# Kernel optimization log

Hardware: AMD Instinct MI355X
Metric: run time of the kernel (lower is better)

Reference implementation:

```python
import jax, jax.numpy as jnp
import numpy as np

N, E, DIN, DOUT = 50000, 625000, 128, 128


def setup_inputs() -> dict:
    key = jax.random.key(0)
    k = jax.random.split(key, 4)
    x = jax.random.normal(k[0], (N, DIN), dtype=jnp.float32)
    edge_index = jax.random.randint(k[1], (2, E), 0, N, dtype=jnp.int32)
    s = 1.0 / np.sqrt(DIN)  # Glorot-ish init like torch Linear
    W_fwd = jax.random.uniform(k[2], (DIN, DOUT), jnp.float32, -s, s)
    W_bwd = jax.random.uniform(k[3], (DIN, DOUT), jnp.float32, -s, s)
    b_fwd = jnp.zeros((DOUT,), jnp.float32)
    b_bwd = jnp.zeros((DOUT,), jnp.float32)
    return {"x": x, "edge_index": edge_index, "W_fwd": W_fwd, "b_fwd": b_fwd,
            "W_bwd": W_bwd, "b_bwd": b_bwd}


def gcn_conv(x, W, b, src, dst, n):
    """PyG GCNConv: add self-loops, symmetric degree norm, gather-scatter aggregate."""
    loops = jnp.arange(n, dtype=src.dtype)
    src2 = jnp.concatenate([src, loops])  # [E+N]
    dst2 = jnp.concatenate([dst, loops])
    ones = jnp.ones(src2.shape[0], dtype=x.dtype)
    deg = jax.ops.segment_sum(ones, dst2, num_segments=n)  # in-degree incl. self-loop
    dinv = jnp.where(deg > 0, jax.lax.rsqrt(deg), 0.0)
    norm = dinv[src2] * dinv[dst2]  # [E+N]
    h = x @ W  # [N, DOUT] dense GEMM before message passing
    msgs = h[src2] * norm[:, None]  # gather + scale, [E+N, DOUT]
    out = jax.ops.segment_sum(msgs, dst2, num_segments=n)  # scatter-add
    return out + b


def reference(x, edge_index, W_fwd, b_fwd, W_bwd, b_bwd):
    src, dst = edge_index[0], edge_index[1]
    n = x.shape[0]
    x_forward = gcn_conv(x, W_fwd, b_fwd, src, dst, n)
    # reversed edge direction for the backward diffusion conv
    x_backward = gcn_conv(x, W_bwd, b_bwd, dst, src, n)
    # dropout omitted (eval mode / deterministic reference)
    return jax.nn.relu(x_forward + x_backward)
```

## Files before the change

kernel.cpp:

```cpp
#include <hip/hip_runtime.h>
#include <hip/hip_bf16.h>
#include <cstdint>

static constexpr int BLK      = 256;
static constexpr int CAP      = 40;
static constexpr int BINSHIFT = 8;
static constexpr int BINNODES = 1 << BINSHIFT;
static constexpr int BINCAP   = BINNODES * CAP / 2;
static constexpr int EPB      = 2048;
static constexpr int OVMAX    = 1024;

typedef __attribute__((ext_vector_type(8))) short bf16x8;
typedef __attribute__((ext_vector_type(4))) float f32x4;

__device__ __forceinline__ float bf16lo(uint32_t u) { return __uint_as_float(u << 16); }
__device__ __forceinline__ float bf16hi(uint32_t u) { return __uint_as_float(u & 0xffff0000u); }
__device__ __forceinline__ unsigned short f2bf(float f) {
    __hip_bfloat16 h = __float2bfloat16(f);
    return *(unsigned short*)&h;
}

__global__ __launch_bounds__(BLK) void k_prep(
        const float* __restrict__ Wf, const float* __restrict__ Wb,
        unsigned short* __restrict__ WTf, unsigned short* __restrict__ WTb,
        int* __restrict__ gcnt, int gcnt_words) {
    const int bid = blockIdx.x;
    if (bid < 8) {
        for (int idx = bid * 2048 + threadIdx.x; idx < (bid + 1) * 2048; idx += BLK) {
            int c = idx >> 7, k = idx & 127;
            WTf[c * 128 + k] = f2bf(Wf[k * 128 + c]);
            WTb[c * 128 + k] = f2bf(Wb[k * 128 + c]);
        }
        return;
    }
    for (int i = threadIdx.x; i < gcnt_words; i += BLK) gcnt[i] = 0;
}

__global__ __launch_bounds__(BLK) void k_bin_gemm(
        const int* __restrict__ src, const int* __restrict__ dst, int ne,
        uint32_t* __restrict__ pair_f, uint32_t* __restrict__ pair_b,
        int* __restrict__ gcnt_f, int* __restrict__ gcnt_b,
        int* __restrict__ ovcnt, int* __restrict__ ovlist,
        const float* __restrict__ x,
        const unsigned short* __restrict__ WTf,
        const unsigned short* __restrict__ WTb,
        unsigned short* __restrict__ h_f, unsigned short* __restrict__ h_b,
        int n, int nbins, int gbin) {
    const int bid = blockIdx.x;
    if (bid < gbin) {
        __shared__ int curf[BINNODES], curb[BINNODES];
        const int tid = threadIdx.x;
        curf[tid] = 0; curb[tid] = 0;
        __syncthreads();

        int s[8], d[8];
        const int e0 = bid * EPB + tid;
#pragma unroll
        for (int k = 0; k < 8; ++k) {
            int e = e0 + k * BLK;
            bool v = e < ne;
            s[k] = v ? src[e] : -1;
            d[k] = v ? dst[e] : -1;
            if (v) {
                atomicAdd(&curf[d[k] >> BINSHIFT], 1);
                atomicAdd(&curb[s[k] >> BINSHIFT], 1);
            }
        }
        __syncthreads();
        int cf = curf[tid], cb = curb[tid];
        if (tid < nbins) {
            curf[tid] = cf ? atomicAdd(&gcnt_f[tid], cf) : 0;
            curb[tid] = cb ? atomicAdd(&gcnt_b[tid], cb) : 0;
        }
        __syncthreads();
#pragma unroll
        for (int k = 0; k < 8; ++k) {
            if (s[k] >= 0) {
                int bf = d[k] >> BINSHIFT;
                int rf = atomicAdd(&curf[bf], 1);
                if (rf < BINCAP)
                    pair_f[(size_t)bf * BINCAP + rf] =
                        ((uint32_t)d[k] << 16) | (uint32_t)s[k];
                else { int q = atomicAdd(ovcnt, 1); if (q < OVMAX) ovlist[q] = (d[k] << 1) | 0; }
                int bb = s[k] >> BINSHIFT;
                int rb = atomicAdd(&curb[bb], 1);
                if (rb < BINCAP)
                    pair_b[(size_t)bb * BINCAP + rb] =
                        ((uint32_t)s[k] << 16) | (uint32_t)d[k];
                else { int q = atomicAdd(ovcnt, 1); if (q < OVMAX) ovlist[q] = (s[k] << 1) | 1; }
            }
        }
        return;
    }
    {
        const int gb   = bid - gbin;
        const int wave = threadIdx.x >> 6;
        const int lane = threadIdx.x & 63;
        const int conv = wave >> 1;
        const int n0   = (wave & 1) * 64;
        const int m0   = gb * 16;
        const int q    = lane >> 4;
        const int t16  = lane & 15;

        const unsigned short* __restrict__ WT = conv ? WTb : WTf;
        unsigned short* __restrict__ h        = conv ? h_b : h_f;

        int arow = m0 + t16; if (arow >= n) arow = n - 1;
        const float* __restrict__ xr = x + (size_t)arow * 128;
        bf16x8 a[4];
#pragma unroll
        for (int s2 = 0; s2 < 4; ++s2) {
            float4 p0v = *(const float4*)(xr + s2 * 32 + q * 8);
            float4 p1v = *(const float4*)(xr + s2 * 32 + q * 8 + 4);
            bf16x8 v;
            v[0] = (short)f2bf(p0v.x); v[1] = (short)f2bf(p0v.y);
            v[2] = (short)f2bf(p0v.z); v[3] = (short)f2bf(p0v.w);
            v[4] = (short)f2bf(p1v.x); v[5] = (short)f2bf(p1v.y);
            v[6] = (short)f2bf(p1v.z); v[7] = (short)f2bf(p1v.w);
            a[s2] = v;
        }
#pragma unroll
        for (int t = 0; t < 4; ++t) {
            const unsigned short* wrow = WT + (size_t)(n0 + t * 16 + t16) * 128;
            f32x4 c = {0.f, 0.f, 0.f, 0.f};
#pragma unroll
            for (int s2 = 0; s2 < 4; ++s2) {
                bf16x8 b = *(const bf16x8*)(wrow + s2 * 32 + q * 8);
                c = __builtin_amdgcn_mfma_f32_16x16x32_bf16(a[s2], b, c, 0, 0, 0);
            }
#pragma unroll
            for (int r = 0; r < 4; ++r) {
                int row = m0 + q * 4 + r;
                if (row < n)
                    h[(size_t)row * 128 + n0 + t * 16 + t16] = f2bf(c[r]);
            }
        }
    }
}

__global__ __launch_bounds__(BLK) void k_build(
        const uint32_t* __restrict__ pair_f, const uint32_t* __restrict__ pair_b,
        const int* __restrict__ gcnt_f, const int* __restrict__ gcnt_b,
        unsigned short* __restrict__ adj_f, unsigned short* __restrict__ adj_b,
        int* __restrict__ cnt_f, int* __restrict__ cnt_b,
        float* __restrict__ dinv_f, float* __restrict__ dinv_b,
        int* __restrict__ ovcnt, int* __restrict__ ovlist,
        int n, int nbins) {
    const int tid = threadIdx.x;
    const int b   = blockIdx.x;
    const int dir = b >= nbins ? 1 : 0;
    const int bin = b - dir * nbins;

    const uint32_t* __restrict__ pairs = dir ? pair_b : pair_f;
    unsigned short* __restrict__ adj   = dir ? adj_b : adj_f;
    int*   cnt  = dir ? cnt_b  : cnt_f;
    float* dinv = dir ? dinv_b : dinv_f;
    int count = dir ? gcnt_b[bin] : gcnt_f[bin];
    if (count > BINCAP) count = BINCAP;

    __shared__ unsigned short buck[BINNODES * CAP];
    __shared__ int lcnt[BINNODES];
    lcnt[tid] = 0;
    __syncthreads();

    const uint32_t* pb = pairs + (size_t)bin * BINCAP;
    for (int i = tid; i < count; i += BLK) {
        uint32_t p = pb[i];
        int l = (p >> 16) & (BINNODES - 1);
        int r = atomicAdd(&lcnt[l], 1);
        if (r < CAP) buck[l * CAP + r] = (unsigned short)(p & 0xffffu);
        else {
            int q = atomicAdd(ovcnt, 1);
            if (q < OVMAX) ovlist[q] = ((((bin << BINSHIFT) + l) << 1) | dir);
        }
    }
    __syncthreads();

    const int node0 = bin << BINSHIFT;
    const int node  = node0 + tid;
    if (node < n) {
        int c = lcnt[tid];
        cnt[node]  = c;
        dinv[node] = rsqrtf(1.0f + (float)c);
    }
    uint32_t* adjseg = (uint32_t*)(adj + (size_t)node0 * CAP);
    const uint32_t* b32 = (const uint32_t*)buck;
    for (int i = tid; i < BINCAP; i += BLK) adjseg[i] = b32[i];
}

__global__ __launch_bounds__(BLK) void k_gatherX(
        const int* __restrict__ cnt_f, const unsigned short* __restrict__ adj_f,
        const int* __restrict__ cnt_b, const unsigned short* __restrict__ adj_b,
        const float* __restrict__ dinv_f, const float* __restrict__ dinv_b,
        const uint32_t* __restrict__ hf, const uint32_t* __restrict__ hb,
        const float* __restrict__ bf, const float* __restrict__ bb,
        float* __restrict__ out, int n, int gnode, int nwords,
        const int* __restrict__ ovcnt, const int* __restrict__ ovlist,
        const int* __restrict__ src, const int* __restrict__ dst, int ne) {
    const int bid = blockIdx.x;
    if (bid < gnode) {
        const int wave = threadIdx.x >> 6;
        const int lane = threadIdx.x & 63;
        const int node = bid * 4 + wave;
        if (node >= n) return;

        int cf = cnt_f[node], cb = cnt_b[node];
        if (cf > CAP || cb > CAP) return;

        float dvsf = dinv_f[node], dvsb = dinv_b[node];
        uint32_t uf = hf[(size_t)node * 64 + lane];
        uint32_t ub = hf[(size_t)(nwords + node * 64 + lane)];
        float acc0 = dvsf * dvsf * bf16lo(uf) + dvsb * dvsb * bf16lo(ub);
        float acc1 = dvsf * dvsf * bf16hi(uf) + dvsb * dvsb * bf16hi(ub);

        const int mt = cf + cb;
        if (mt <= 64) {
            int ofs = 0; float sc = 0.f;
            if (lane < cf) {
                int nb = adj_f[node * CAP + lane];
                ofs = nb * 64;
                sc  = dvsf * dinv_f[nb];
            } else if (lane < mt) {
                int nb = adj_b[node * CAP + (lane - cf)];
                ofs = nwords + nb * 64;
                sc  = dvsb * dinv_b[nb];
            }
            int j = 0;
            for (; j + 8 <= mt; j += 8) {
                int   o0 = __shfl(ofs, j + 0), o1 = __shfl(ofs, j + 1);
                int   o2 = __shfl(ofs, j + 2), o3 = __shfl(ofs, j + 3);
                int   o4 = __shfl(ofs, j + 4), o5 = __shfl(ofs, j + 5);
                int   o6 = __shfl(ofs, j + 6), o7 = __shfl(ofs, j + 7);
                float s0 = __shfl(sc, j + 0), s1 = __shfl(sc, j + 1);
                float s2 = __shfl(sc, j + 2), s3 = __shfl(sc, j + 3);
                float s4 = __shfl(sc, j + 4), s5 = __shfl(sc, j + 5);
                float s6 = __shfl(sc, j + 6), s7 = __shfl(sc, j + 7);
                uint32_t u0 = hf[(size_t)(o0 + lane)];
                uint32_t u1 = hf[(size_t)(o1 + lane)];
                uint32_t u2 = hf[(size_t)(o2 + lane)];
                uint32_t u3 = hf[(size_t)(o3 + lane)];
                uint32_t u4 = hf[(size_t)(o4 + lane)];
                uint32_t u5 = hf[(size_t)(o5 + lane)];
                uint32_t u6 = hf[(size_t)(o6 + lane)];
                uint32_t u7 = hf[(size_t)(o7 + lane)];
                acc0 = fmaf(s0, bf16lo(u0), acc0); acc1 = fmaf(s0, bf16hi(u0), acc1);
                acc0 = fmaf(s1, bf16lo(u1), acc0); acc1 = fmaf(s1, bf16hi(u1), acc1);
                acc0 = fmaf(s2, bf16lo(u2), acc0); acc1 = fmaf(s2, bf16hi(u2), acc1);
                acc0 = fmaf(s3, bf16lo(u3), acc0); acc1 = fmaf(s3, bf16hi(u3), acc1);
                acc0 = fmaf(s4, bf16lo(u4), acc0); acc1 = fmaf(s4, bf16hi(u4), acc1);
                acc0 = fmaf(s5, bf16lo(u5), acc0); acc1 = fmaf(s5, bf16hi(u5), acc1);
                acc0 = fmaf(s6, bf16lo(u6), acc0); acc1 = fmaf(s6, bf16hi(u6), acc1);
                acc0 = fmaf(s7, bf16lo(u7), acc0); acc1 = fmaf(s7, bf16hi(u7), acc1);
            }
            for (; j + 4 <= mt; j += 4) {
                int   o0 = __shfl(ofs, j + 0), o1 = __shfl(ofs, j + 1);
                int   o2 = __shfl(ofs, j + 2), o3 = __shfl(ofs, j + 3);
                float s0 = __shfl(sc, j + 0), s1 = __shfl(sc, j + 1);
                float s2 = __shfl(sc, j + 2), s3 = __shfl(sc, j + 3);
                uint32_t u0 = hf[(size_t)(o0 + lane)];
                uint32_t u1 = hf[(size_t)(o1 + lane)];
                uint32_t u2 = hf[(size_t)(o2 + lane)];
                uint32_t u3 = hf[(size_t)(o3 + lane)];
                acc0 = fmaf(s0, bf16lo(u0), acc0); acc1 = fmaf(s0, bf16hi(u0), acc1);
                acc0 = fmaf(s1, bf16lo(u1), acc0); acc1 = fmaf(s1, bf16hi(u1), acc1);
                acc0 = fmaf(s2, bf16lo(u2), acc0); acc1 = fmaf(s2, bf16hi(u2), acc1);
                acc0 = fmaf(s3, bf16lo(u3), acc0); acc1 = fmaf(s3, bf16hi(u3), acc1);
            }
            for (; j < mt; ++j) {
                int oj = __shfl(ofs, j); float sj = __shfl(sc, j);
                uint32_t uj = hf[(size_t)(oj + lane)];
                acc0 = fmaf(sj, bf16lo(uj), acc0); acc1 = fmaf(sj, bf16hi(uj), acc1);
            }
        } else {
            for (int j = 0; j < cf; ++j) {
                int nb = adj_f[node * CAP + j];
                float dj = dvsf * dinv_f[nb];
                uint32_t u = hf[(size_t)nb * 64 + lane];
                acc0 = fmaf(dj, bf16lo(u), acc0); acc1 = fmaf(dj, bf16hi(u), acc1);
            }
            for (int j = 0; j < cb; ++j) {
                int nb = adj_b[node * CAP + j];
                float dj = dvsb * dinv_b[nb];
                uint32_t u = hf[(size_t)(nwords + nb * 64 + lane)];
                acc0 = fmaf(dj, bf16lo(u), acc0); acc1 = fmaf(dj, bf16hi(u), acc1);
            }
        }

        const float2 biasf = ((const float2*)bf)[lane];
        const float2 biasb = ((const float2*)bb)[lane];
        float v0 = acc0 + biasf.x + biasb.x;
        float v1 = acc1 + biasf.y + biasb.y;
        ((float2*)out)[(size_t)node * 64 + lane] =
            make_float2(fmaxf(v0, 0.0f), fmaxf(v1, 0.0f));
        return;
    }

    int nov = *ovcnt; if (nov > OVMAX) nov = OVMAX;
    if (nov == 0) return;
    __shared__ int lst[4096];
    __shared__ int lcnt;
    const int tid = threadIdx.x;
    for (int i = bid - gnode; i < nov; i += 8) {
        int code = ovlist[i];
        int node = code >> 1;
        float acc0 = 0.f, acc1 = 0.f;
        for (int d2 = 0; d2 < 2; ++d2) {
            const int* key = d2 ? src : dst;
            const int* val = d2 ? dst : src;
            const float* dinv = d2 ? dinv_b : dinv_f;
            int base = d2 ? nwords : 0;
            float dvs = dinv[node];
            float s0 = 0.f, s1 = 0.f;
            if (tid < 64) {
                uint32_t u = hf[(size_t)(base + node * 64 + tid)];
                s0 = dvs * bf16lo(u); s1 = dvs * bf16hi(u);
            }
            for (int start = 0; start < ne; start += 4096) {
                if (tid == 0) lcnt = 0;
                __syncthreads();
                int end = min(start + 4096, ne);
                for (int e2 = start + tid; e2 < end; e2 += BLK)
                    if (key[e2] == node) { int q = atomicAdd(&lcnt, 1); lst[q] = val[e2]; }
                __syncthreads();
                int mm = lcnt;
                if (tid < 64) {
                    for (int j = 0; j < mm; ++j) {
                        int nb = lst[j];
                        float dv = dinv[nb];
                        uint32_t u = hf[(size_t)(base + nb * 64 + tid)];
                        s0 = fmaf(dv, bf16lo(u), s0);
                        s1 = fmaf(dv, bf16hi(u), s1);
                    }
                }
                __syncthreads();
            }
            if (tid < 64) { acc0 += dvs * s0; acc1 += dvs * s1; }
        }
        if (tid < 64) {
            float2 biasf = ((const float2*)bf)[tid];
            float2 biasb = ((const float2*)bb)[tid];
            float v0 = acc0 + biasf.x + biasb.x;
            float v1 = acc1 + biasf.y + biasb.y;
            ((float2*)out)[(size_t)node * 64 + tid] =
                make_float2(fmaxf(v0, 0.0f), fmaxf(v1, 0.0f));
        }
        __syncthreads();
    }
}

extern "C" void kernel_launch(void* const* d_in, const int* in_sizes, int n_in,
                              void* d_out, int out_size, void* d_ws, size_t ws_size,
                              hipStream_t stream) {
    const float* x  = (const float*)d_in[0];
    const int*   ei = (const int*)d_in[1];
    const float* Wf = (const float*)d_in[2];
    const float* bf = (const float*)d_in[3];
    const float* Wb = (const float*)d_in[4];
    const float* bb = (const float*)d_in[5];

    const int n  = in_sizes[0] / 128;
    const int ne = in_sizes[1] / 2;
    const int* src = ei;
    const int* dst = ei + ne;
    float* out = (float*)d_out;

    const int nbins = (n + BINNODES - 1) >> BINSHIFT;

    char* w = (char*)d_ws;
    unsigned short* h_f = (unsigned short*)w;   w += (size_t)n * 128 * 2;
    unsigned short* h_b = (unsigned short*)w;   w += (size_t)n * 128 * 2;
    uint32_t* pair_f = (uint32_t*)w;            w += (size_t)nbins * BINCAP * 4;
    uint32_t* pair_b = (uint32_t*)w;            w += (size_t)nbins * BINCAP * 4;
    float* dinv_f = (float*)w;                  w += (size_t)n * 4;
    float* dinv_b = (float*)w;                  w += (size_t)n * 4;
    unsigned short* WTf = (unsigned short*)w;   w += 128 * 128 * 2;
    unsigned short* WTb = (unsigned short*)w;   w += 128 * 128 * 2;
    int* cnt_f = (int*)w;                       w += (size_t)n * 4;
    int* cnt_b = (int*)w;                       w += (size_t)n * 4;
    int* gcnt_f = (int*)w;                      w += (size_t)nbins * 4;
    int* gcnt_b = (int*)w;                      w += (size_t)nbins * 4;
    int* ovcnt = (int*)w;                       w += 8 * 4;
    int* ovlist = (int*)w;                      w += OVMAX * 4;

    unsigned short* adj_f = (unsigned short*)pair_f;
    unsigned short* adj_b = (unsigned short*)pair_b;

    const int gbin  = (ne + EPB - 1) / EPB;
    const int gg    = (n + 15) / 16;
    const int gnode = (n + 3) / 4;

    k_prep<<<9, BLK, 0, stream>>>(Wf, Wb, WTf, WTb, gcnt_f, 2 * nbins + 8);

    k_bin_gemm<<<gbin + gg, BLK, 0, stream>>>(src, dst, ne,
                                              pair_f, pair_b, gcnt_f, gcnt_b,
                                              ovcnt, ovlist,
                                              x, WTf, WTb, h_f, h_b,
                                              n, nbins, gbin);

    k_build<<<2 * nbins, BLK, 0, stream>>>(pair_f, pair_b, gcnt_f, gcnt_b,
                                           adj_f, adj_b, cnt_f, cnt_b,
                                           dinv_f, dinv_b, ovcnt, ovlist,
                                           n, nbins);

    k_gatherX<<<gnode + 8, BLK, 0, stream>>>(cnt_f, adj_f, cnt_b, adj_b,
                                             dinv_f, dinv_b,
                                             (const uint32_t*)h_f,
                                             (const uint32_t*)h_b,
                                             bf, bb, out, n, gnode, n * 64,
                                             ovcnt, ovlist, src, dst, ne);
}
```

Measured before the change: 191.6 us.

## Aggregate raw features before GEMM and stage binned edges in shared memory

Reorders the computation to aggregate bf16-converted x over neighbours first, writing both direction aggregates as bf16 into the output buffer. A single fused GEMM with K=256 then applies both weight matrices, bias and ReLU. The gather now reads one shared feature table instead of two projected tables. The binning kernel sorts edges per block in shared memory by prefix sum so global pair writes are contiguous. The costs are an extra GEMM pass that reads back the aggregate, bf16 rounding of the aggregates, and a binary search per staged element.

```diff
diff --git a/kernel.cpp b/kernel.cpp
--- a/kernel.cpp
+++ b/kernel.cpp
@@ -9,6 +9,7 @@
 static constexpr int BINCAP   = BINNODES * CAP / 2;
 static constexpr int EPB      = 2048;
 static constexpr int OVMAX    = 1024;
+static constexpr int NB2MAX   = 512;
 
 typedef __attribute__((ext_vector_type(8))) short bf16x8;
 typedef __attribute__((ext_vector_type(4))) float f32x4;
@@ -20,181 +21,197 @@
     return *(unsigned short*)&h;
 }
 
-__global__ __launch_bounds__(BLK) void k_prep(
-        const float* __restrict__ Wf, const float* __restrict__ Wb,
-        unsigned short* __restrict__ WTf, unsigned short* __restrict__ WTb,
-        int* __restrict__ gcnt, int gcnt_words) {
-    const int bid = blockIdx.x;
-    if (bid < 8) {
-        for (int idx = bid * 2048 + threadIdx.x; idx < (bid + 1) * 2048; idx += BLK) {
-            int c = idx >> 7, k = idx & 127;
-            WTf[c * 128 + k] = f2bf(Wf[k * 128 + c]);
-            WTb[c * 128 + k] = f2bf(Wb[k * 128 + c]);
-        }
-        return;
-    }
-    for (int i = threadIdx.x; i < gcnt_words; i += BLK) gcnt[i] = 0;
-}
-
-__global__ __launch_bounds__(BLK) void k_bin_gemm(
+__global__ __launch_bounds__(BLK) void k_bin(
         const int* __restrict__ src, const int* __restrict__ dst, int ne,
-        uint32_t* __restrict__ pair_f, uint32_t* __restrict__ pair_b,
-        int* __restrict__ gcnt_f, int* __restrict__ gcnt_b,
-        int* __restrict__ ovcnt, int* __restrict__ ovlist,
-        const float* __restrict__ x,
-        const unsigned short* __restrict__ WTf,
-        const unsigned short* __restrict__ WTb,
-        unsigned short* __restrict__ h_f, unsigned short* __restrict__ h_b,
-        int n, int nbins, int gbin) {
-    const int bid = blockIdx.x;
-    if (bid < gbin) {
-        __shared__ int curf[BINNODES], curb[BINNODES];
-        const int tid = threadIdx.x;
-        curf[tid] = 0; curb[tid] = 0;
-        __syncthreads();
-
-        int s[8], d[8];
-        const int e0 = bid * EPB + tid;
-#pragma unroll
-        for (int k = 0; k < 8; ++k) {
-            int e = e0 + k * BLK;
-            bool v = e < ne;
-            s[k] = v ? src[e] : -1;
-            d[k] = v ? dst[e] : -1;
-            if (v) {
-                atomicAdd(&curf[d[k] >> BINSHIFT], 1);
-                atomicAdd(&curb[s[k] >> BINSHIFT], 1);
-            }
-        }
-        __syncthreads();
-        int cf = curf[tid], cb = curb[tid];
-        if (tid < nbins) {
-            curf[tid] = cf ? atomicAdd(&gcnt_f[tid], cf) : 0;
-            curb[tid] = cb ? atomicAdd(&gcnt_b[tid], cb) : 0;
-        }
-        __syncthreads();
-#pragma unroll
-        for (int k = 0; k < 8; ++k) {
-            if (s[k] >= 0) {
-                int bf = d[k] >> BINSHIFT;
-                int rf = atomicAdd(&curf[bf], 1);
-                if (rf < BINCAP)
-                    pair_f[(size_t)bf * BINCAP + rf] =
-                        ((uint32_t)d[k] << 16) | (uint32_t)s[k];
-                else { int q = atomicAdd(ovcnt, 1); if (q < OVMAX) ovlist[q] = (d[k] << 1) | 0; }
-                int bb = s[k] >> BINSHIFT;
-                int rb = atomicAdd(&curb[bb], 1);
-                if (rb < BINCAP)
-                    pair_b[(size_t)bb * BINCAP + rb] =
-                        ((uint32_t)s[k] << 16) | (uint32_t)d[k];
-                else { int q = atomicAdd(ovcnt, 1); if (q < OVMAX) ovlist[q] = (s[k] << 1) | 1; }
-            }
-        }
-        return;
-    }
-    {
-        const int gb   = bid - gbin;
-        const int wave = threadIdx.x >> 6;
-        const int lane = threadIdx.x & 63;
-        const int conv = wave >> 1;
-        const int n0   = (wave & 1) * 64;
-        const int m0   = gb * 16;
-        const int q    = lane >> 4;
-        const int t16  = lane & 15;
-
-        const unsigned short* __restrict__ WT = conv ? WTb : WTf;
-        unsigned short* __restrict__ h        = conv ? h_b : h_f;
-
-        int arow = m0 + t16; if (arow >= n) arow = n - 1;
-        const float* __restrict__ xr = x + (size_t)arow * 128;
-        bf16x8 a[4];
-#pragma unroll
-        for (int s2 = 0; s2 < 4; ++s2) {
-            float4 p0v = *(const float4*)(xr + s2 * 32 + q * 8);
-            float4 p1v = *(const float4*)(xr + s2 * 32 + q * 8 + 4);
-            bf16x8 v;
-            v[0] = (short)f2bf(p0v.x); v[1] = (short)f2bf(p0v.y);
-            v[2] = (short)f2bf(p0v.z); v[3] = (short)f2bf(p0v.w);
-            v[4] = (short)f2bf(p1v.x); v[5] = (short)f2bf(p1v.y);
-            v[6] = (short)f2bf(p1v.z); v[7] = (short)f2bf(p1v.w);
-            a[s2] = v;
-        }
-#pragma unroll
-        for (int t = 0; t < 4; ++t) {
-            const unsigned short* wrow = WT + (size_t)(n0 + t * 16 + t16) * 128;
-            f32x4 c = {0.f, 0.f, 0.f, 0.f};
-#pragma unroll
-            for (int s2 = 0; s2 < 4; ++s2) {
-                bf16x8 b = *(const bf16x8*)(wrow + s2 * 32 + q * 8);
-                c = __builtin_amdgcn_mfma_f32_16x16x32_bf16(a[s2], b, c, 0, 0, 0);
-            }
-#pragma unroll
-            for (int r = 0; r < 4; ++r) {
-                int row = m0 + q * 4 + r;
-                if (row < n)
-                    h[(size_t)row * 128 + n0 + t * 16 + t16] = f2bf(c[r]);
-            }
-        }
-    }
-}
-
-__global__ __launch_bounds__(BLK) void k_build(
-        const uint32_t* __restrict__ pair_f, const uint32_t* __restrict__ pair_b,
-        const int* __restrict__ gcnt_f, const int* __restrict__ gcnt_b,
-        unsigned short* __restrict__ adj_f, unsigned short* __restrict__ adj_b,
+        uint32_t* __restrict__ pair, int* __restrict__ gcnt,
+        int* __restrict__ ovcnt, int* __restrict__ ovlist, int nbins) {
+    __shared__ uint32_t stage[EPB * 2];
+    __shared__ int hist[NB2MAX];
+    __shared__ int lofs[NB2MAX];
+    __shared__ int gbase[NB2MAX];
+    __shared__ int chunk[NB2MAX / 8];
+    const int tid = threadIdx.x, bid = blockIdx.x;
+    const int nb2 = 2 * nbins;
+    for (int i = tid; i < nb2; i += BLK) hist[i] = 0;
+    __syncthreads();
+
+    int s[8], d[8];
+    const int e0 = bid * EPB + tid;
+#pragma unroll
+    for (int k = 0; k < 8; ++k) {
+        int e = e0 + k * BLK;
+        bool v = e < ne;
+        s[k] = v ? src[e] : -1;
+        d[k] = v ? dst[e] : -1;
+        if (v) {
+            atomicAdd(&hist[d[k] >> BINSHIFT], 1);
+            atomicAdd(&hist[nbins + (s[k] >> BINSHIFT)], 1);
+        }
+    }
+    __syncthreads();
+
+    const int nch = (nb2 + 7) >> 3;
+    if (tid < nch) {
+        int a = 0, base = tid << 3;
+#pragma unroll
+        for (int k = 0; k < 8; ++k) { int idx = base + k; if (idx < nb2) a += hist[idx]; }
+        chunk[tid] = a;
+    }
+    __syncthreads();
+    if (tid == 0) { int a = 0; for (int c = 0; c < nch; ++c) { int t = chunk[c]; chunk[c] = a; a += t; } }
+    __syncthreads();
+    for (int i = tid; i < nb2; i += BLK) {
+        int a = chunk[i >> 3];
+        for (int k = (i >> 3) << 3; k < i; ++k) a += hist[k];
+        lofs[i] = a;
+    }
+    __syncthreads();
+    for (int i = tid; i < nb2; i += BLK) {
+        int c = hist[i];
+        gbase[i] = c ? atomicAdd(&gcnt[i], c) : 0;
+        hist[i] = lofs[i];
+    }
+    __syncthreads();
+#pragma unroll
+    for (int k = 0; k < 8; ++k) {
+        if (s[k] >= 0) {
+            int b0 = d[k] >> BINSHIFT;
+            int p0 = atomicAdd(&hist[b0], 1);
+            stage[p0] = ((uint32_t)d[k] << 16) | (uint32_t)s[k];
+            int b1 = nbins + (s[k] >> BINSHIFT);
+            int p1 = atomicAdd(&hist[b1], 1);
+            stage[p1] = ((uint32_t)s[k] << 16) | (uint32_t)d[k];
+        }
+    }
+    __syncthreads();
+    int nval = ne - bid * EPB; if (nval > EPB) nval = EPB; if (nval < 0) nval = 0;
+    const int total = 2 * nval;
+    for (int i = tid; i < total; i += BLK) {
+        int lo = 0, hi = nb2 - 1;
+        while (lo < hi) { int mid = (lo + hi + 1) >> 1; if (lofs[mid] <= i) lo = mid; else hi = mid - 1; }
+        int gidx = gbase[lo] + (i - lofs[lo]);
+        if (gidx < BINCAP)
+            pair[(size_t)lo * BINCAP + gidx] = stage[i];
+        else {
+            int node = (int)(stage[i] >> 16);
+            int q = atomicAdd(ovcnt, 1);
+            if (q < OVMAX) ovlist[q] = (node << 1) | (lo >= nbins ? 1 : 0);
+        }
+    }
+}
+
+__global__ __launch_bounds__(BLK) void k_build_conv(
+        uint32_t* __restrict__ pair, const int* __restrict__ gcnt,
         int* __restrict__ cnt_f, int* __restrict__ cnt_b,
         float* __restrict__ dinv_f, float* __restrict__ dinv_b,
         int* __restrict__ ovcnt, int* __restrict__ ovlist,
+        const float* __restrict__ x, uint32_t* __restrict__ xb32, int nxw, int gxc,
+        const float* __restrict__ Wf, const float* __restrict__ Wb,
+        unsigned short* __restrict__ WTf, unsigned short* __restrict__ WTb,
         int n, int nbins) {
-    const int tid = threadIdx.x;
-    const int b   = blockIdx.x;
-    const int dir = b >= nbins ? 1 : 0;
-    const int bin = b - dir * nbins;
-
-    const uint32_t* __restrict__ pairs = dir ? pair_b : pair_f;
-    unsigned short* __restrict__ adj   = dir ? adj_b : adj_f;
-    int*   cnt  = dir ? cnt_b  : cnt_f;
-    float* dinv = dir ? dinv_b : dinv_f;
-    int count = dir ? gcnt_b[bin] : gcnt_f[bin];
-    if (count > BINCAP) count = BINCAP;
-
-    __shared__ unsigned short buck[BINNODES * CAP];
-    __shared__ int lcnt[BINNODES];
-    lcnt[tid] = 0;
-    __syncthreads();
-
-    const uint32_t* pb = pairs + (size_t)bin * BINCAP;
-    for (int i = tid; i < count; i += BLK) {
-        uint32_t p = pb[i];
-        int l = (p >> 16) & (BINNODES - 1);
-        int r = atomicAdd(&lcnt[l], 1);
-        if (r < CAP) buck[l * CAP + r] = (unsigned short)(p & 0xffffu);
-        else {
-            int q = atomicAdd(ovcnt, 1);
-            if (q < OVMAX) ovlist[q] = ((((bin << BINSHIFT) + l) << 1) | dir);
-        }
-    }
-    __syncthreads();
-
-    const int node0 = bin << BINSHIFT;
-    const int node  = node0 + tid;
-    if (node < n) {
-        int c = lcnt[tid];
-        cnt[node]  = c;
-        dinv[node] = rsqrtf(1.0f + (float)c);
-    }
-    uint32_t* adjseg = (uint32_t*)(adj + (size_t)node0 * CAP);
-    const uint32_t* b32 = (const uint32_t*)buck;
-    for (int i = tid; i < BINCAP; i += BLK) adjseg[i] = b32[i];
-}
-
-__global__ __launch_bounds__(BLK) void k_gatherX(
-        const int* __restrict__ cnt_f, const unsigned short* __restrict__ adj_f,
-        const int* __restrict__ cnt_b, const unsigned short* __restrict__ adj_b,
+    const int bid = blockIdx.x, tid = threadIdx.x;
+    const int nb2 = 2 * nbins;
+    if (bid < nb2) {
+        __shared__ unsigned short buck[BINNODES * CAP];
+        __shared__ int lcnt[BINNODES];
+        lcnt[tid] = 0;
+        __syncthreads();
+        int count = gcnt[bid]; if (count > BINCAP) count = BINCAP;
+        const uint32_t* pb = pair + (size_t)bid * BINCAP;
+        const int dir = bid >= nbins ? 1 : 0;
+        for (int i = tid; i < count; i += BLK) {
+            uint32_t p = pb[i];
+            int l = (p >> 16) & (BINNODES - 1);
+            int r = atomicAdd(&lcnt[l], 1);
+            if (r < CAP) buck[l * CAP + r] = (unsigned short)(p & 0xffffu);
+            else {
+                int q = atomicAdd(ovcnt, 1);
+                if (q < OVMAX)
+                    ovlist[q] = (((((bid - dir * nbins) << BINSHIFT) + l)) << 1) | dir;
+            }
+        }
+        __syncthreads();
+        const int node = ((bid - dir * nbins) << BINSHIFT) + tid;
+        if (node < n) {
+            int c = lcnt[tid];
+            if (dir) { cnt_b[node] = c; dinv_b[node] = rsqrtf(1.0f + (float)c); }
+            else     { cnt_f[node] = c; dinv_f[node] = rsqrtf(1.0f + (float)c); }
+        }
+        uint32_t* seg = pair + (size_t)bid * BINCAP;
+        const uint32_t* b32 = (const uint32_t*)buck;
+        for (int i = tid; i < BINCAP; i += BLK) seg[i] = b32[i];
+        return;
+    }
+    if (bid < nb2 + gxc) {
+        int base = (bid - nb2) * 2048;
+        int end = base + 2048; if (end > nxw) end = nxw;
+        for (int i = base + tid; i < end; i += BLK) {
+            float2 v = ((const float2*)x)[i];
+            xb32[i] = ((uint32_t)f2bf(v.y) << 16) | (uint32_t)f2bf(v.x);
+        }
+        return;
+    }
+    int wb = bid - nb2 - gxc;
+    for (int idx = wb * 2048 + tid; idx < (wb + 1) * 2048; idx += BLK) {
+        int c = idx >> 7, k = idx & 127;
+        WTf[c * 128 + k] = f2bf(Wf[k * 128 + c]);
+        WTb[c * 128 + k] = f2bf(Wb[k * 128 + c]);
+    }
+}
+
+__device__ __forceinline__ void accum_range(
+        int j0, int j1, int ofs, float sc,
+        const uint32_t* __restrict__ xb, int lane, float& a0, float& a1) {
+    int j = j0;
+    for (; j + 8 <= j1; j += 8) {
+        int   o0 = __shfl(ofs, j + 0), o1 = __shfl(ofs, j + 1);
+        int   o2 = __shfl(ofs, j + 2), o3 = __shfl(ofs, j + 3);
+        int   o4 = __shfl(ofs, j + 4), o5 = __shfl(ofs, j + 5);
+        int   o6 = __shfl(ofs, j + 6), o7 = __shfl(ofs, j + 7);
+        float s0 = __shfl(sc, j + 0), s1 = __shfl(sc, j + 1);
+        float s2 = __shfl(sc, j + 2), s3 = __shfl(sc, j + 3);
+        float s4 = __shfl(sc, j + 4), s5 = __shfl(sc, j + 5);
+        float s6 = __shfl(sc, j + 6), s7 = __shfl(sc, j + 7);
+        uint32_t u0 = xb[(size_t)(o0 + lane)], u1 = xb[(size_t)(o1 + lane)];
+        uint32_t u2 = xb[(size_t)(o2 + lane)], u3 = xb[(size_t)(o3 + lane)];
+        uint32_t u4 = xb[(size_t)(o4 + lane)], u5 = xb[(size_t)(o5 + lane)];
+        uint32_t u6 = xb[(size_t)(o6 + lane)], u7 = xb[(size_t)(o7 + lane)];
+        a0 = fmaf(s0, bf16lo(u0), a0); a1 = fmaf(s0, bf16hi(u0), a1);
+        a0 = fmaf(s1, bf16lo(u1), a0); a1 = fmaf(s1, bf16hi(u1), a1);
+        a0 = fmaf(s2, bf16lo(u2), a0); a1 = fmaf(s2, bf16hi(u2), a1);
+        a0 = fmaf(s3, bf16lo(u3), a0); a1 = fmaf(s3, bf16hi(u3), a1);
+        a0 = fmaf(s4, bf16lo(u4), a0); a1 = fmaf(s4, bf16hi(u4), a1);
+        a0 = fmaf(s5, bf16lo(u5), a0); a1 = fmaf(s5, bf16hi(u5), a1);
+        a0 = fmaf(s6, bf16lo(u6), a0); a1 = fmaf(s6, bf16hi(u6), a1);
+        a0 = fmaf(s7, bf16lo(u7), a0); a1 = fmaf(s7, bf16hi(u7), a1);
+    }
+    for (; j + 4 <= j1; j += 4) {
+        int   o0 = __shfl(ofs, j + 0), o1 = __shfl(ofs, j + 1);
+        int   o2 = __shfl(ofs, j + 2), o3 = __shfl(ofs, j + 3);
+        float s0 = __shfl(sc, j + 0), s1 = __shfl(sc, j + 1);
+        float s2 = __shfl(sc, j + 2), s3 = __shfl(sc, j + 3);
+        uint32_t u0 = xb[(size_t)(o0 + lane)], u1 = xb[(size_t)(o1 + lane)];
+        uint32_t u2 = xb[(size_t)(o2 + lane)], u3 = xb[(size_t)(o3 + lane)];
+        a0 = fmaf(s0, bf16lo(u0), a0); a1 = fmaf(s0, bf16hi(u0), a1);
+        a0 = fmaf(s1, bf16lo(u1), a0); a1 = fmaf(s1, bf16hi(u1), a1);
+        a0 = fmaf(s2, bf16lo(u2), a0); a1 = fmaf(s2, bf16hi(u2), a1);
+        a0 = fmaf(s3, bf16lo(u3), a0); a1 = fmaf(s3, bf16hi(u3), a1);
+    }
+    for (; j < j1; ++j) {
+        int oj = __shfl(ofs, j); float sj = __shfl(sc, j);
+        uint32_t uj = xb[(size_t)(oj + lane)];
+        a0 = fmaf(sj, bf16lo(uj), a0); a1 = fmaf(sj, bf16hi(uj), a1);
+    }
+}
+
+__global__ __launch_bounds__(BLK) void k_gather_agg(
+        const int* __restrict__ cnt_f, const int* __restrict__ cnt_b,
+        const unsigned short* __restrict__ adj_f,
+        const unsigned short* __restrict__ adj_b,
         const float* __restrict__ dinv_f, const float* __restrict__ dinv_b,
-        const uint32_t* __restrict__ hf, const uint32_t* __restrict__ hb,
-        const float* __restrict__ bf, const float* __restrict__ bb,
-        float* __restrict__ out, int n, int gnode, int nwords,
+        const uint32_t* __restrict__ xb32,
+        uint32_t* __restrict__ agg32,
+        int n, int gnode,
         const int* __restrict__ ovcnt, const int* __restrict__ ovlist,
         const int* __restrict__ src, const int* __restrict__ dst, int ne) {
     const int bid = blockIdx.x;
@@ -208,10 +225,9 @@
         if (cf > CAP || cb > CAP) return;
 
         float dvsf = dinv_f[node], dvsb = dinv_b[node];
-        uint32_t uf = hf[(size_t)node * 64 + lane];
-        uint32_t ub = hf[(size_t)(nwords + node * 64 + lane)];
-        float acc0 = dvsf * dvsf * bf16lo(uf) + dvsb * dvsb * bf16lo(ub);
-        float acc1 = dvsf * dvsf * bf16hi(uf) + dvsb * dvsb * bf16hi(ub);
+        uint32_t uv = xb32[(size_t)node * 64 + lane];
+        float accf0 = dvsf * dvsf * bf16lo(uv), accf1 = dvsf * dvsf * bf16hi(uv);
+        float accb0 = dvsb * dvsb * bf16lo(uv), accb1 = dvsb * dvsb * bf16hi(uv);
 
         const int mt = cf + cb;
         if (mt <= 64) {
@@ -222,129 +238,118 @@
                 sc  = dvsf * dinv_f[nb];
             } else if (lane < mt) {
                 int nb = adj_b[node * CAP + (lane - cf)];
-                ofs = nwords + nb * 64;
+                ofs = nb * 64;
                 sc  = dvsb * dinv_b[nb];
             }
-            int j = 0;
-            for (; j + 8 <= mt; j += 8) {
-                int   o0 = __shfl(ofs, j + 0), o1 = __shfl(ofs, j + 1);
-                int   o2 = __shfl(ofs, j + 2), o3 = __shfl(ofs, j + 3);
-                int   o4 = __shfl(ofs, j + 4), o5 = __shfl(ofs, j + 5);
-                int   o6 = __shfl(ofs, j + 6), o7 = __shfl(ofs, j + 7);
-                float s0 = __shfl(sc, j + 0), s1 = __shfl(sc, j + 1);
-                float s2 = __shfl(sc, j + 2), s3 = __shfl(sc, j + 3);
-                float s4 = __shfl(sc, j + 4), s5 = __shfl(sc, j + 5);
-                float s6 = __shfl(sc, j + 6), s7 = __shfl(sc, j + 7);
-                uint32_t u0 = hf[(size_t)(o0 + lane)];
-                uint32_t u1 = hf[(size_t)(o1 + lane)];
-                uint32_t u2 = hf[(size_t)(o2 + lane)];
-                uint32_t u3 = hf[(size_t)(o3 + lane)];
-                uint32_t u4 = hf[(size_t)(o4 + lane)];
-                uint32_t u5 = hf[(size_t)(o5 + lane)];
-                uint32_t u6 = hf[(size_t)(o6 + lane)];
-                uint32_t u7 = hf[(size_t)(o7 + lane)];
-                acc0 = fmaf(s0, bf16lo(u0), acc0); acc1 = fmaf(s0, bf16hi(u0), acc1);
-                acc0 = fmaf(s1, bf16lo(u1), acc0); acc1 = fmaf(s1, bf16hi(u1), acc1);
-                acc0 = fmaf(s2, bf16lo(u2), acc0); acc1 = fmaf(s2, bf16hi(u2), acc1);
-                acc0 = fmaf(s3, bf16lo(u3), acc0); acc1 = fmaf(s3, bf16hi(u3), acc1);
-                acc0 = fmaf(s4, bf16lo(u4), acc0); acc1 = fmaf(s4, bf16hi(u4), acc1);
-                acc0 = fmaf(s5, bf16lo(u5), acc0); acc1 = fmaf(s5, bf16hi(u5), acc1);
-                acc0 = fmaf(s6, bf16lo(u6), acc0); acc1 = fmaf(s6, bf16hi(u6), acc1);
-                acc0 = fmaf(s7, bf16lo(u7), acc0); acc1 = fmaf(s7, bf16hi(u7), acc1);
-            }
-            for (; j + 4 <= mt; j += 4) {
-                int   o0 = __shfl(ofs, j + 0), o1 = __shfl(ofs, j + 1);
-                int   o2 = __shfl(ofs, j + 2), o3 = __shfl(ofs, j + 3);
-                float s0 = __shfl(sc, j + 0), s1 = __shfl(sc, j + 1);
-                float s2 = __shfl(sc, j + 2), s3 = __shfl(sc, j + 3);
-                uint32_t u0 = hf[(size_t)(o0 + lane)];
-                uint32_t u1 = hf[(size_t)(o1 + lane)];
-                uint32_t u2 = hf[(size_t)(o2 + lane)];
-                uint32_t u3 = hf[(size_t)(o3 + lane)];
-                acc0 = fmaf(s0, bf16lo(u0), acc0); acc1 = fmaf(s0, bf16hi(u0), acc1);
-                acc0 = fmaf(s1, bf16lo(u1), acc0); acc1 = fmaf(s1, bf16hi(u1), acc1);
-                acc0 = fmaf(s2, bf16lo(u2), acc0); acc1 = fmaf(s2, bf16hi(u2), acc1);
-                acc0 = fmaf(s3, bf16lo(u3), acc0); acc1 = fmaf(s3, bf16hi(u3), acc1);
-            }
-            for (; j < mt; ++j) {
-                int oj = __shfl(ofs, j); float sj = __shfl(sc, j);
-                uint32_t uj = hf[(size_t)(oj + lane)];
-                acc0 = fmaf(sj, bf16lo(uj), acc0); acc1 = fmaf(sj, bf16hi(uj), acc1);
-            }
+            accum_range(0,  cf, ofs, sc, xb32, lane, accf0, accf1);
+            accum_range(cf, mt, ofs, sc, xb32, lane, accb0, accb1);
         } else {
             for (int j = 0; j < cf; ++j) {
                 int nb = adj_f[node * CAP + j];
                 float dj = dvsf * dinv_f[nb];
-                uint32_t u = hf[(size_t)nb * 64 + lane];
-                acc0 = fmaf(dj, bf16lo(u), acc0); acc1 = fmaf(dj, bf16hi(u), acc1);
+                uint32_t u = xb32[(size_t)nb * 64 + lane];
+                accf0 = fmaf(dj, bf16lo(u), accf0); accf1 = fmaf(dj, bf16hi(u), accf1);
             }
             for (int j = 0; j < cb; ++j) {
                 int nb = adj_b[node * CAP + j];
                 float dj = dvsb * dinv_b[nb];
-                uint32_t u = hf[(size_t)(nwords + nb * 64 + lane)];
-                acc0 = fmaf(dj, bf16lo(u), acc0); acc1 = fmaf(dj, bf16hi(u), acc1);
-            }
-        }
-
-        const float2 biasf = ((const float2*)bf)[lane];
-        const float2 biasb = ((const float2*)bb)[lane];
-        float v0 = acc0 + biasf.x + biasb.x;
-        float v1 = acc1 + biasf.y + biasb.y;
-        ((float2*)out)[(size_t)node * 64 + lane] =
-            make_float2(fmaxf(v0, 0.0f), fmaxf(v1, 0.0f));
+                uint32_t u = xb32[(size_t)nb * 64 + lane];
+                accb0 = fmaf(dj, bf16lo(u), accb0); accb1 = fmaf(dj, bf16hi(u), accb1);
+            }
+        }
+        agg32[(size_t)node * 128 + lane] =
+            ((uint32_t)f2bf(accf1) << 16) | (uint32_t)f2bf(accf0);
+        agg32[(size_t)node * 128 + 64 + lane] =
+            ((uint32_t)f2bf(accb1) << 16) | (uint32_t)f2bf(accb0);
         return;
     }
 
     int nov = *ovcnt; if (nov > OVMAX) nov = OVMAX;
     if (nov == 0) return;
     __shared__ int lst[4096];
-    __shared__ int lcnt;
+    __shared__ int lc;
     const int tid = threadIdx.x;
     for (int i = bid - gnode; i < nov; i += 8) {
-        int code = ovlist[i];
-        int node = code >> 1;
-        float acc0 = 0.f, acc1 = 0.f;
+        int node = ovlist[i] >> 1;
         for (int d2 = 0; d2 < 2; ++d2) {
             const int* key = d2 ? src : dst;
             const int* val = d2 ? dst : src;
             const float* dinv = d2 ? dinv_b : dinv_f;
-            int base = d2 ? nwords : 0;
             float dvs = dinv[node];
             float s0 = 0.f, s1 = 0.f;
             if (tid < 64) {
-                uint32_t u = hf[(size_t)(base + node * 64 + tid)];
+                uint32_t u = xb32[(size_t)node * 64 + tid];
                 s0 = dvs * bf16lo(u); s1 = dvs * bf16hi(u);
             }
             for (int start = 0; start < ne; start += 4096) {
-                if (tid == 0) lcnt = 0;
+                if (tid == 0) lc = 0;
                 __syncthreads();
                 int end = min(start + 4096, ne);
                 for (int e2 = start + tid; e2 < end; e2 += BLK)
-                    if (key[e2] == node) { int q = atomicAdd(&lcnt, 1); lst[q] = val[e2]; }
+                    if (key[e2] == node) { int q = atomicAdd(&lc, 1); lst[q] = val[e2]; }
                 __syncthreads();
-                int mm = lcnt;
+                int mm = lc;
                 if (tid < 64) {
                     for (int j = 0; j < mm; ++j) {
                         int nb = lst[j];
                         float dv = dinv[nb];
-                        uint32_t u = hf[(size_t)(base + nb * 64 + tid)];
+                        uint32_t u = xb32[(size_t)nb * 64 + tid];
                         s0 = fmaf(dv, bf16lo(u), s0);
                         s1 = fmaf(dv, bf16hi(u), s1);
                     }
                 }
                 __syncthreads();
             }
-            if (tid < 64) { acc0 += dvs * s0; acc1 += dvs * s1; }
-        }
-        if (tid < 64) {
-            float2 biasf = ((const float2*)bf)[tid];
-            float2 biasb = ((const float2*)bb)[tid];
-            float v0 = acc0 + biasf.x + biasb.x;
-            float v1 = acc1 + biasf.y + biasb.y;
-            ((float2*)out)[(size_t)node * 64 + tid] =
-                make_float2(fmaxf(v0, 0.0f), fmaxf(v1, 0.0f));
-        }
-        __syncthreads();
+            if (tid < 64) {
+                float a0 = dvs * s0, a1 = dvs * s1;
+                agg32[(size_t)node * 128 + d2 * 64 + tid] =
+                    ((uint32_t)f2bf(a1) << 16) | (uint32_t)f2bf(a0);
+            }
+            __syncthreads();
+        }
+    }
+}
+
+__global__ __launch_bounds__(BLK) void k_gemm_out(
+        const unsigned short* __restrict__ agg,
+        const unsigned short* __restrict__ WTf,
+        const unsigned short* __restrict__ WTb,
+        const float* __restrict__ bfv, const float* __restrict__ bbv,
+        float* __restrict__ out, int n) {
+    const int wave = threadIdx.x >> 6, lane = threadIdx.x & 63;
+    const int wm = wave >> 1, wh = wave & 1;
+    const int q = lane >> 4, t16 = lane & 15;
+    const int m0 = blockIdx.x * 32 + wm * 16;
+    int arow = m0 + t16; if (arow >= n) arow = n - 1;
+    const unsigned short* ra = agg + (size_t)arow * 256;
+    bf16x8 af[4], ab[4];
+#pragma unroll
+    for (int s = 0; s < 4; ++s) {
+        af[s] = *(const bf16x8*)(ra + s * 32 + q * 8);
+        ab[s] = *(const bf16x8*)(ra + 128 + s * 32 + q * 8);
+    }
+    __syncthreads();
+#pragma unroll
+    for (int t = 0; t < 4; ++t) {
+        const int col = wh * 64 + t * 16 + t16;
+        const unsigned short* wrf = WTf + (size_t)col * 128;
+        const unsigned short* wrb = WTb + (size_t)col * 128;
+        f32x4 c = {0.f, 0.f, 0.f, 0.f};
+#pragma unroll
+        for (int s = 0; s < 4; ++s)
+            c = __builtin_amdgcn_mfma_f32_16x16x32_bf16(
+                    af[s], *(const bf16x8*)(wrf + s * 32 + q * 8), c, 0, 0, 0);
+#pragma unroll
+        for (int s = 0; s < 4; ++s)
+            c = __builtin_amdgcn_mfma_f32_16x16x32_bf16(
+                    ab[s], *(const bf16x8*)(wrb + s * 32 + q * 8), c, 0, 0, 0);
+        const float bias = bfv[col] + bbv[col];
+#pragma unroll
+        for (int r = 0; r < 4; ++r) {
+            int row = m0 + q * 4 + r;
+            if (row < n)
+                out[(size_t)row * 128 + col] = fmaxf(c[r] + bias, 0.f);
+        }
     }
 }
 
@@ -365,47 +370,45 @@
     float* out = (float*)d_out;
 
     const int nbins = (n + BINNODES - 1) >> BINSHIFT;
+    const int nb2   = 2 * nbins;
 
     char* w = (char*)d_ws;
-    unsigned short* h_f = (unsigned short*)w;   w += (size_t)n * 128 * 2;
-    unsigned short* h_b = (unsigned short*)w;   w += (size_t)n * 128 * 2;
-    uint32_t* pair_f = (uint32_t*)w;            w += (size_t)nbins * BINCAP * 4;
-    uint32_t* pair_b = (uint32_t*)w;            w += (size_t)nbins * BINCAP * 4;
+    uint32_t* pair = (uint32_t*)w;              w += (size_t)nb2 * BINCAP * 4;
+    uint32_t* xb32 = (uint32_t*)w;              w += (size_t)n * 64 * 4;
     float* dinv_f = (float*)w;                  w += (size_t)n * 4;
     float* dinv_b = (float*)w;                  w += (size_t)n * 4;
     unsigned short* WTf = (unsigned short*)w;   w += 128 * 128 * 2;
     unsigned short* WTb = (unsigned short*)w;   w += 128 * 128 * 2;
     int* cnt_f = (int*)w;                       w += (size_t)n * 4;
     int* cnt_b = (int*)w;                       w += (size_t)n * 4;
-    int* gcnt_f = (int*)w;                      w += (size_t)nbins * 4;
-    int* gcnt_b = (int*)w;                      w += (size_t)nbins * 4;
+    int* gcnt = (int*)w;                        w += (size_t)nb2 * 4;
     int* ovcnt = (int*)w;                       w += 8 * 4;
     int* ovlist = (int*)w;                      w += OVMAX * 4;
 
-    unsigned short* adj_f = (unsigned short*)pair_f;
-    unsigned short* adj_b = (unsigned short*)pair_b;
+    const unsigned short* adj_f = (const unsigned short*)pair;
+    const unsigned short* adj_b = adj_f + (size_t)nbins * BINNODES * CAP;
+    uint32_t* agg32 = (uint32_t*)d_out;
 
     const int gbin  = (ne + EPB - 1) / EPB;
-    const int gg    = (n + 15) / 16;
+    const int gxc   = (n * 64 + 2047) / 2048;
     const int gnode = (n + 3) / 4;
-
-    k_prep<<<9, BLK, 0, stream>>>(Wf, Wb, WTf, WTb, gcnt_f, 2 * nbins + 8);
-
-    k_bin_gemm<<<gbin + gg, BLK, 0, stream>>>(src, dst, ne,
-                                              pair_f, pair_b, gcnt_f, gcnt_b,
-                                              ovcnt, ovlist,
-                                              x, WTf, WTb, h_f, h_b,
-                                              n, nbins, gbin);
-
-    k_build<<<2 * nbins, BLK, 0, stream>>>(pair_f, pair_b, gcnt_f, gcnt_b,
-                                           adj_f, adj_b, cnt_f, cnt_b,
-                                           dinv_f, dinv_b, ovcnt, ovlist,
-                                           n, nbins);
-
-    k_gatherX<<<gnode + 8, BLK, 0, stream>>>(cnt_f, adj_f, cnt_b, adj_b,
-                                             dinv_f, dinv_b,
-                                             (const uint32_t*)h_f,
-                                             (const uint32_t*)h_b,
-                                             bf, bb, out, n, gnode, n * 64,
-                                             ovcnt, ovlist, src, dst, ne);
-}
+    const int ggo   = (n + 31) / 32;
+
+    hipMemsetAsync(gcnt, 0, (size_t)(nb2 + 8) * 4, stream);
+
+    k_bin<<<gbin, BLK, 0, stream>>>(src, dst, ne, pair, gcnt, ovcnt, ovlist, nbins);
+
+    k_build_conv<<<nb2 + gxc + 8, BLK, 0, stream>>>(pair, gcnt,
+                                                    cnt_f, cnt_b, dinv_f, dinv_b,
+                                                    ovcnt, ovlist,
+                                                    x, xb32, n * 64, gxc,
+                                                    Wf, Wb, WTf, WTb, n, nbins);
+
+    k_gather_agg<<<gnode + 8, BLK, 0, stream>>>(cnt_f, cnt_b, adj_f, adj_b,
+                                                dinv_f, dinv_b, xb32,
+                                                agg32, n, gnode,
+                                                ovcnt, ovlist, src, dst, ne);
+
+    k_gemm_out<<<ggo, BLK, 0, stream>>>((const unsigned short*)agg32,
+                                        WTf, WTb, bf, bb, out, n);
+}
```

After: 199.4 us. +4.0%, slower.
